# Optimization experiments

Hardware: AMD Instinct MI355X
Metric: run time of the kernel (lower is better)

The kernel has to match this reference:

```python
import jax, jax.numpy as jnp
import numpy as np

M_CHK, N_VAR, DV = 576, 1152, 3  # (3,x)-regular-column LDPC, rate 1/2
PI = 3.1415926


def _build_bp_matrices():
    """Vectorized replica of GetMatrixForBPNet (same math, no Python O(E^2) loops)."""
    rng = np.random.default_rng(0)
    H = np.zeros((M_CHK, N_VAR), np.float32)
    rows = np.argsort(rng.random((N_VAR, M_CHK)), axis=1)[:, :DV]  # DV distinct rows per column
    H[rows.ravel(), np.repeat(np.arange(N_VAR), DV)] = 1.0
    ii, jj = np.nonzero(H)                 # row-major edge list (sorted by row, then col)
    E = ii.size
    p_r2l = np.lexsort((ii, jj))           # Map_row_to_line: col-major position -> row-major index
    p_l2r = np.argsort(p_r2l)              # Map_line_to_row: inverse permutation
    cols_cm = jj[p_r2l]                    # column of each edge in col-major ("line") order
    # variable-node sum excluding self, in col-major order, then permute row-major input -> col-major
    S_V = (cols_cm[:, None] == cols_cm[None, :]).astype(np.float32)
    np.fill_diagonal(S_V, 0.0)
    H_sumV_to_C = np.zeros((E, E), np.float32)
    H_sumV_to_C[:, p_r2l] = S_V
    # check-node sum excluding self, in row-major order, then permute col-major input -> row-major
    S_C = (ii[:, None] == ii[None, :]).astype(np.float32)
    np.fill_diagonal(S_C, 0.0)
    H_sumC_to_V = np.zeros((E, E), np.float32)
    H_sumC_to_V[:, p_l2r] = S_C
    # llr -> per-edge init (col-major order)
    H_x_to_xe0 = np.zeros((E, N_VAR), np.float32)
    H_x_to_xe0[np.arange(E), cols_cm] = 1.0
    # per-variable sum of final edge messages (row-major input -> col-major sum)
    A = (np.arange(N_VAR)[:, None] == cols_cm[None, :]).astype(np.float32)
    H_xe_v_sumc_to_y = np.zeros((N_VAR, E), np.float32)
    H_xe_v_sumc_to_y[:, p_r2l] = A
    return H_x_to_xe0, H_sumC_to_V, H_sumV_to_C, H_xe_v_sumc_to_y


def setup_inputs() -> dict:
    key = jax.random.key(0)
    H_x_to_xe0, H_sumC_to_V, H_sumV_to_C, H_xe_v_sumc_to_y = _build_bp_matrices()
    llr_in = 2.0 * jax.random.normal(key, (16, N_VAR), dtype=jnp.float32)
    return {
        "llr_in": llr_in,
        "H_x_to_xe0": jnp.asarray(H_x_to_xe0),
        "H_sumC_to_V": jnp.asarray(H_sumC_to_V),
        "H_sumV_to_C": jnp.asarray(H_sumV_to_C),
        "H_xe_v_sumc_to_y": jnp.asarray(H_xe_v_sumc_to_y),
        "bp_iter_num": 8,
    }


def _one_bp_iteration(xe_v2c, xe_0, H_sumC_to_V, H_sumV_to_C):
    xe_tanh = jnp.tanh(xe_v2c / 2.0)
    sgn = jnp.sign(xe_tanh)
    # log-domain product over check-node neighbors (excluding self) via complex log trick
    sum_log_img = H_sumC_to_V @ ((1.0 - sgn) * (0.5 * PI))
    sum_log_real = H_sumC_to_V @ jnp.log(1e-8 + jnp.abs(xe_tanh))
    xe_product = jnp.exp(sum_log_real) * jnp.cos(sum_log_img)  # Re(exp(r + i*theta))
    xe_pd = xe_product + jnp.sign(xe_product) * (-2e-7)
    # 2 * atanh(x) with the module's custom atanh = 0.5*log((1+x)/(1-x+1e-10))
    xe_v_sumc = jnp.log((1.0 + xe_pd) / (1.0 - xe_pd + 1e-10))
    xe_c_sumv = xe_0 + H_sumV_to_C @ xe_v_sumc
    return xe_v_sumc, xe_c_sumv


def reference(llr_in, H_x_to_xe0, H_sumC_to_V, H_sumV_to_C, H_xe_v_sumc_to_y, bp_iter_num):
    llr_t = llr_in.T                      # [n, batch]
    xe_0 = H_x_to_xe0 @ llr_t             # [E, batch]
    xe_v2c = xe_0
    for _ in range(bp_iter_num - 1):
        _, xe_v2c = _one_bp_iteration(xe_v2c, xe_0, H_sumC_to_V, H_sumV_to_C)
    xe_v_sumc, _ = _one_bp_iteration(xe_v2c, xe_0, H_sumC_to_V, H_sumV_to_C)
    bp_out_llr = llr_t + H_xe_v_sumc_to_y @ xe_v_sumc
    dec_out = (1 - jnp.sign(bp_out_llr).astype(jnp.int32)) // 2
    return dec_out.T
```

## Files before the change

kernel.cpp:

```cpp
#include <hip/hip_runtime.h>

#define NV 1152
#define MC 576
#define NE 3456
#define RPG 36
#define GRP 16
#define EMAX 384

__global__ __launch_bounds__(256) void k_tri(const float* __restrict__ Hy,
                                             int* __restrict__ tri) {
    __shared__ int found[8];
    __shared__ int cnt;
    const int v = blockIdx.x, t = threadIdx.x;
    if (t == 0) cnt = 0;
    __syncthreads();
    const float4* row4 = (const float4*)(Hy + (size_t)v * NE);
    for (int c = t; c < 864; c += 256) {
        float4 q = row4[c];
        if (q.x != 0.0f) { int s = atomicAdd(&cnt, 1); if (s < 8) found[s] = 4 * c; }
        if (q.y != 0.0f) { int s = atomicAdd(&cnt, 1); if (s < 8) found[s] = 4 * c + 1; }
        if (q.z != 0.0f) { int s = atomicAdd(&cnt, 1); if (s < 8) found[s] = 4 * c + 2; }
        if (q.w != 0.0f) { int s = atomicAdd(&cnt, 1); if (s < 8) found[s] = 4 * c + 3; }
    }
    __syncthreads();
    if (t == 0) {
        int a = found[0], b = found[1], c = found[2];
        int lo = min(a, min(b, c));
        int hi = max(a, max(b, c));
        int mid = a + b + c - lo - hi;
        tri[3 * v] = lo; tri[3 * v + 1] = mid; tri[3 * v + 2] = hi;
    }
}

__global__ __launch_bounds__(1024) void k_build(const float* __restrict__ Hc,
                                                const int* __restrict__ tri,
                                                unsigned short* __restrict__ pl2r_g,
                                                int* __restrict__ rs_g) {
    __shared__ unsigned short pl2r[NE];
    __shared__ unsigned short flg[NE];
    __shared__ int wtot[16];
    const int t = threadIdx.x;
    const int lane = t & 63, wid = t >> 6;
    for (int r = t; r < MC + 1; r += 1024) rs_g[r] = NE;
    for (int e = t; e < NE; e += 1024) pl2r[tri[e]] = (unsigned short)e;
    __syncthreads();
    for (int a = t; a < NE; a += 1024) {
        int fl = 0;
        if (a > 0) fl = (Hc[(size_t)(a - 1) * NE + (int)pl2r[a]] == 0.0f) ? 1 : 0;
        flg[a] = (unsigned short)fl;
        pl2r_g[a] = pl2r[a];
    }
    __syncthreads();
    int inc[4];
    int run = 0;
    const int base4 = t * 4;
    #pragma unroll
    for (int k = 0; k < 4; k++) {
        int idx = base4 + k;
        run += (idx < NE) ? (int)flg[idx] : 0;
        inc[k] = run;
    }
    int x = run;
    #pragma unroll
    for (int d = 1; d < 64; d <<= 1) {
        int y = __shfl_up(x, d, 64);
        if (lane >= d) x += y;
    }
    if (lane == 63) wtot[wid] = x;
    __syncthreads();
    if (t < 16) {
        int v = wtot[t];
        #pragma unroll
        for (int d = 1; d < 16; d <<= 1) {
            int y = __shfl_up(v, d, 16);
            if (t >= d) v += y;
        }
        wtot[t] = v;
    }
    __syncthreads();
    const int prefix = ((wid > 0) ? wtot[wid - 1] : 0) + (x - run);
    #pragma unroll
    for (int k = 0; k < 4; k++) {
        int idx = base4 + k;
        if (idx < NE) {
            int rid = prefix + inc[k];
            if (idx == 0 || flg[idx]) rs_g[rid] = idx;
        }
    }
}

__global__ __launch_bounds__(256) void k_iter(const float* __restrict__ llr,
                                              const unsigned short* __restrict__ p_l2r,
                                              const int* __restrict__ rs,
                                              const float* __restrict__ msg_in,
                                              float* __restrict__ msg_out,
                                              int first) {
    __shared__ float2 lrli[EMAX];
    __shared__ unsigned short eloc[EMAX];
    __shared__ unsigned char rloc[EMAX];
    __shared__ int rsl[RPG + 1];
    const int g = blockIdx.x, b = blockIdx.y, t = threadIdx.x;
    if (t <= RPG) rsl[t] = rs[g * RPG + t];
    __syncthreads();
    const int s0 = rsl[0], s1 = rsl[RPG];
    for (int a = s0 + t; a < s1; a += 256) {
        int la = a - s0;
        int lo = 0, hi = RPG - 1;
        while (lo < hi) { int mid = (lo + hi + 1) >> 1; if (rsl[mid] <= a) lo = mid; else hi = mid - 1; }
        rloc[la] = (unsigned char)lo;
        int e = p_l2r[a];
        eloc[la] = (unsigned short)e;
        int v = e / 3;
        float xv = llr[b * NV + v];
        if (!first) {
            int v3 = 3 * v, r_ = e - v3;
            int o1 = v3 + ((r_ == 0) ? 1 : 0);
            int o2 = v3 + ((r_ == 2) ? 1 : 2);
            xv = xv + (msg_in[b * NE + o1] + msg_in[b * NE + o2]);
        }
        float tv = tanhf(0.5f * xv);
        float sgn = (tv > 0.0f) ? 1.0f : ((tv < 0.0f) ? -1.0f : 0.0f);
        lrli[la] = make_float2(logf(1e-8f + fabsf(tv)),
                               (1.0f - sgn) * 1.5707963f);
    }
    __syncthreads();
    for (int a = s0 + t; a < s1; a += 256) {
        int la = a - s0;
        int r = rloc[la];
        int js = rsl[r] - s0, je = rsl[r + 1] - s0;
        float slr = 0.0f, sli = 0.0f;
        for (int j = js; j < je; ++j) {
            if (j != la) { float2 q = lrli[j]; slr += q.x; sli += q.y; }
        }
        float p = expf(slr) * cosf(sli);
        float ps = (p > 0.0f) ? 1.0f : ((p < 0.0f) ? -1.0f : 0.0f);
        float pd = p - 2e-7f * ps;
        msg_out[b * NE + eloc[la]] = logf((1.0f + pd) / ((1.0f - pd) + 1e-10f));
    }
}

__global__ void k_out(const float* __restrict__ llr, const float* __restrict__ msg,
                      int* __restrict__ out, int n) {
    int i = blockIdx.x * 256 + threadIdx.x;
    if (i >= n) return;
    int b = i / NV, v = i - b * NV;
    const float* m = msg + (size_t)b * NE + 3 * v;
    float S = (m[0] + m[1]) + m[2];
    out[i] = ((llr[i] + S) < 0.0f) ? 1 : 0;
}

extern "C" void kernel_launch(void* const* d_in, const int* in_sizes, int n_in,
                              void* d_out, int out_size, void* d_ws, size_t ws_size,
                              hipStream_t stream) {
    const float* llr_in = (const float*)d_in[0];
    const float* Hc2v   = (const float*)d_in[2];
    const float* Hy     = (const float*)d_in[4];
    const int batch = in_sizes[0] / NV;
    int* tri = (int*)d_ws;
    int* rs  = tri + NE;
    float* msgA = (float*)(rs + 580);
    float* msgB = msgA + (size_t)batch * NE;
    unsigned short* pl2r = (unsigned short*)(msgB + (size_t)batch * NE);

    hipLaunchKernelGGL(k_tri, dim3(NV), dim3(256), 0, stream, Hy, tri);
    hipLaunchKernelGGL(k_build, dim3(1), dim3(1024), 0, stream, Hc2v, tri, pl2r, rs);
    hipLaunchKernelGGL(k_iter, dim3(GRP, batch), dim3(256), 0, stream,
                       llr_in, pl2r, rs, msgA, msgA, 1);
    float* bufs[2] = { msgA, msgB };
    for (int it = 1; it < 8; ++it) {
        float* in  = bufs[(it + 1) & 1];
        float* out = bufs[it & 1];
        hipLaunchKernelGGL(k_iter, dim3(GRP, batch), dim3(256), 0, stream,
                           llr_in, pl2r, rs, in, out, 0);
    }
    const int n = batch * NV;
    hipLaunchKernelGGL(k_out, dim3((n + 255) / 256), dim3(256), 0, stream,
                       llr_in, msgB, (int*)d_out, n);
}
```

Baseline: 180.3 us.

## Fuse all BP stages into one cooperative persistent kernel with grid barriers

Replaces the separate launches (edge-finding, structure build, eight iteration launches and output) with a single cooperative kernel of GRP*batch blocks. Grid-wide atomic barriers separate the setup phases, and per-batch counters synchronise the 16 blocks that share a codeword between iterations. The per-block edge metadata and llr values are loaded into shared memory once and reused across all iterations. This removes about ten kernel launch gaps but adds spin-barrier overhead, a memset, and serialised setup, since only 256 blocks now scan the large Hy matrix.

```diff
diff --git a/kernel.cpp b/kernel.cpp
--- a/kernel.cpp
+++ b/kernel.cpp
@@ -7,99 +7,111 @@
 #define GRP 16
 #define EMAX 384
 
-__global__ __launch_bounds__(256) void k_tri(const float* __restrict__ Hy,
-                                             int* __restrict__ tri) {
-    __shared__ int found[8];
-    __shared__ int cnt;
-    const int v = blockIdx.x, t = threadIdx.x;
-    if (t == 0) cnt = 0;
+__device__ __forceinline__ void wait_bar(int* c, int target) {
     __syncthreads();
-    const float4* row4 = (const float4*)(Hy + (size_t)v * NE);
-    for (int c = t; c < 864; c += 256) {
-        float4 q = row4[c];
-        if (q.x != 0.0f) { int s = atomicAdd(&cnt, 1); if (s < 8) found[s] = 4 * c; }
-        if (q.y != 0.0f) { int s = atomicAdd(&cnt, 1); if (s < 8) found[s] = 4 * c + 1; }
-        if (q.z != 0.0f) { int s = atomicAdd(&cnt, 1); if (s < 8) found[s] = 4 * c + 2; }
-        if (q.w != 0.0f) { int s = atomicAdd(&cnt, 1); if (s < 8) found[s] = 4 * c + 3; }
+    if (threadIdx.x == 0) {
+        __hip_atomic_fetch_add(c, 1, __ATOMIC_ACQ_REL, __HIP_MEMORY_SCOPE_AGENT);
+        while (__hip_atomic_load(c, __ATOMIC_ACQUIRE, __HIP_MEMORY_SCOPE_AGENT) < target)
+            __builtin_amdgcn_s_sleep(1);
     }
     __syncthreads();
-    if (t == 0) {
-        int a = found[0], b = found[1], c = found[2];
-        int lo = min(a, min(b, c));
-        int hi = max(a, max(b, c));
-        int mid = a + b + c - lo - hi;
-        tri[3 * v] = lo; tri[3 * v + 1] = mid; tri[3 * v + 2] = hi;
-    }
 }
 
-__global__ __launch_bounds__(1024) void k_build(const float* __restrict__ Hc,
-                                                const int* __restrict__ tri,
-                                                unsigned short* __restrict__ pl2r_g,
-                                                int* __restrict__ rs_g) {
-    __shared__ unsigned short pl2r[NE];
-    __shared__ unsigned short flg[NE];
-    __shared__ int wtot[16];
-    const int t = threadIdx.x;
-    const int lane = t & 63, wid = t >> 6;
-    for (int r = t; r < MC + 1; r += 1024) rs_g[r] = NE;
-    for (int e = t; e < NE; e += 1024) pl2r[tri[e]] = (unsigned short)e;
-    __syncthreads();
-    for (int a = t; a < NE; a += 1024) {
-        int fl = 0;
-        if (a > 0) fl = (Hc[(size_t)(a - 1) * NE + (int)pl2r[a]] == 0.0f) ? 1 : 0;
-        flg[a] = (unsigned short)fl;
-        pl2r_g[a] = pl2r[a];
-    }
-    __syncthreads();
-    int inc[4];
-    int run = 0;
-    const int base4 = t * 4;
-    #pragma unroll
-    for (int k = 0; k < 4; k++) {
-        int idx = base4 + k;
-        run += (idx < NE) ? (int)flg[idx] : 0;
-        inc[k] = run;
-    }
-    int x = run;
-    #pragma unroll
-    for (int d = 1; d < 64; d <<= 1) {
-        int y = __shfl_up(x, d, 64);
-        if (lane >= d) x += y;
-    }
-    if (lane == 63) wtot[wid] = x;
-    __syncthreads();
-    if (t < 16) {
-        int v = wtot[t];
-        #pragma unroll
-        for (int d = 1; d < 16; d <<= 1) {
-            int y = __shfl_up(v, d, 16);
-            if (t >= d) v += y;
-        }
-        wtot[t] = v;
-    }
-    __syncthreads();
-    const int prefix = ((wid > 0) ? wtot[wid - 1] : 0) + (x - run);
-    #pragma unroll
-    for (int k = 0; k < 4; k++) {
-        int idx = base4 + k;
-        if (idx < NE) {
-            int rid = prefix + inc[k];
-            if (idx == 0 || flg[idx]) rs_g[rid] = idx;
-        }
-    }
-}
+#define GCNT(i)     (cnt + (i) * 16)
+#define BCNT(b, it) (cnt + (3 + (b) * 8 + (it)) * 16)
 
-__global__ __launch_bounds__(256) void k_iter(const float* __restrict__ llr,
-                                              const unsigned short* __restrict__ p_l2r,
-                                              const int* __restrict__ rs,
-                                              const float* __restrict__ msg_in,
-                                              float* __restrict__ msg_out,
-                                              int first) {
+__global__ __launch_bounds__(256) void k_bp(const float* __restrict__ llr,
+                                            const float* __restrict__ Hc,
+                                            const float* __restrict__ Hy,
+                                            unsigned short* __restrict__ pl2r,
+                                            int* __restrict__ rs,
+                                            unsigned char* __restrict__ flg,
+                                            float* __restrict__ msgA,
+                                            float* __restrict__ msgB,
+                                            int* __restrict__ cnt,
+                                            int* __restrict__ out) {
+    const int bid = blockIdx.x, t = threadIdx.x;
+    const int nblk = gridDim.x;
+    __shared__ int found[8];
+    __shared__ int fcnt;
+    __shared__ int wtot[4];
+    __shared__ int rsl[RPG + 1];
     __shared__ float2 lrli[EMAX];
     __shared__ unsigned short eloc[EMAX];
     __shared__ unsigned char rloc[EMAX];
-    __shared__ int rsl[RPG + 1];
-    const int g = blockIdx.x, b = blockIdx.y, t = threadIdx.x;
+    __shared__ float xb[EMAX];
+
+    for (int v = bid; v < NV; v += nblk) {
+        if (t == 0) fcnt = 0;
+        __syncthreads();
+        const float4* row4 = (const float4*)(Hy + (size_t)v * NE);
+        for (int c4 = t; c4 < 864; c4 += 256) {
+            float4 q = row4[c4];
+            if (q.x != 0.0f) { int s = atomicAdd(&fcnt, 1); if (s < 8) found[s] = 4 * c4; }
+            if (q.y != 0.0f) { int s = atomicAdd(&fcnt, 1); if (s < 8) found[s] = 4 * c4 + 1; }
+            if (q.z != 0.0f) { int s = atomicAdd(&fcnt, 1); if (s < 8) found[s] = 4 * c4 + 2; }
+            if (q.w != 0.0f) { int s = atomicAdd(&fcnt, 1); if (s < 8) found[s] = 4 * c4 + 3; }
+        }
+        __syncthreads();
+        if (t == 0) {
+            int a = found[0], b2 = found[1], c2 = found[2];
+            int lo = min(a, min(b2, c2));
+            int hi = max(a, max(b2, c2));
+            int mid = a + b2 + c2 - lo - hi;
+            pl2r[lo]  = (unsigned short)(3 * v);
+            pl2r[mid] = (unsigned short)(3 * v + 1);
+            pl2r[hi]  = (unsigned short)(3 * v + 2);
+        }
+        __syncthreads();
+    }
+    wait_bar(GCNT(0), nblk);
+
+    {
+        int gt = bid * 256 + t;
+        if (gt <= MC) rs[gt] = NE;
+        if (gt < NE) {
+            int fl = 0;
+            if (gt > 0) fl = (Hc[(size_t)(gt - 1) * NE + (int)pl2r[gt]] == 0.0f) ? 1 : 0;
+            flg[gt] = (unsigned char)fl;
+        }
+    }
+    wait_bar(GCNT(1), nblk);
+
+    if (bid == 0) {
+        const int lane = t & 63, wid = t >> 6;
+        int inc[14];
+        int run = 0;
+        const int base = t * 14;
+        #pragma unroll
+        for (int k = 0; k < 14; k++) {
+            int idx = base + k;
+            run += (idx < NE) ? (int)flg[idx] : 0;
+            inc[k] = run;
+        }
+        int x = run;
+        #pragma unroll
+        for (int d = 1; d < 64; d <<= 1) {
+            int y = __shfl_up(x, d, 64);
+            if (lane >= d) x += y;
+        }
+        if (lane == 63) wtot[wid] = x;
+        __syncthreads();
+        if (t == 0) {
+            int s = 0;
+            #pragma unroll
+            for (int w = 0; w < 4; w++) { int v = wtot[w]; wtot[w] = s; s += v; }
+        }
+        __syncthreads();
+        const int prefix = wtot[wid] + (x - run);
+        #pragma unroll
+        for (int k = 0; k < 14; k++) {
+            int idx = base + k;
+            if (idx < NE && (idx == 0 || flg[idx])) rs[prefix + inc[k]] = idx;
+        }
+    }
+    wait_bar(GCNT(2), nblk);
+
+    const int g = bid & 15, b = bid >> 4;
     if (t <= RPG) rsl[t] = rs[g * RPG + t];
     __syncthreads();
     const int s0 = rsl[0], s1 = rsl[RPG];
@@ -108,45 +120,54 @@
         int lo = 0, hi = RPG - 1;
         while (lo < hi) { int mid = (lo + hi + 1) >> 1; if (rsl[mid] <= a) lo = mid; else hi = mid - 1; }
         rloc[la] = (unsigned char)lo;
-        int e = p_l2r[a];
+        int e = pl2r[a];
         eloc[la] = (unsigned short)e;
-        int v = e / 3;
-        float xv = llr[b * NV + v];
-        if (!first) {
-            int v3 = 3 * v, r_ = e - v3;
-            int o1 = v3 + ((r_ == 0) ? 1 : 0);
-            int o2 = v3 + ((r_ == 2) ? 1 : 2);
-            xv = xv + (msg_in[b * NE + o1] + msg_in[b * NE + o2]);
-        }
-        float tv = tanhf(0.5f * xv);
-        float sgn = (tv > 0.0f) ? 1.0f : ((tv < 0.0f) ? -1.0f : 0.0f);
-        lrli[la] = make_float2(logf(1e-8f + fabsf(tv)),
-                               (1.0f - sgn) * 1.5707963f);
+        xb[la] = llr[b * NV + e / 3];
     }
     __syncthreads();
-    for (int a = s0 + t; a < s1; a += 256) {
-        int la = a - s0;
-        int r = rloc[la];
-        int js = rsl[r] - s0, je = rsl[r + 1] - s0;
-        float slr = 0.0f, sli = 0.0f;
-        for (int j = js; j < je; ++j) {
-            if (j != la) { float2 q = lrli[j]; slr += q.x; sli += q.y; }
+
+    for (int it = 0; it < 8; ++it) {
+        const float* mi = (it & 1) ? msgA : msgB;
+        float* mo       = (it & 1) ? msgB : msgA;
+        for (int a = s0 + t; a < s1; a += 256) {
+            int la = a - s0;
+            int e = eloc[la];
+            float xv = xb[la];
+            if (it > 0) {
+                int v3 = 3 * (e / 3), r_ = e - v3;
+                int o1 = v3 + ((r_ == 0) ? 1 : 0);
+                int o2 = v3 + ((r_ == 2) ? 1 : 2);
+                xv = xv + (mi[b * NE + o1] + mi[b * NE + o2]);
+            }
+            float tv = tanhf(0.5f * xv);
+            float sgn = (tv > 0.0f) ? 1.0f : ((tv < 0.0f) ? -1.0f : 0.0f);
+            lrli[la] = make_float2(logf(1e-8f + fabsf(tv)),
+                                   (1.0f - sgn) * 1.5707963f);
         }
-        float p = expf(slr) * cosf(sli);
-        float ps = (p > 0.0f) ? 1.0f : ((p < 0.0f) ? -1.0f : 0.0f);
-        float pd = p - 2e-7f * ps;
-        msg_out[b * NE + eloc[la]] = logf((1.0f + pd) / ((1.0f - pd) + 1e-10f));
+        __syncthreads();
+        for (int a = s0 + t; a < s1; a += 256) {
+            int la = a - s0;
+            int r = rloc[la];
+            int js = rsl[r] - s0, je = rsl[r + 1] - s0;
+            float slr = 0.0f, sli = 0.0f;
+            for (int j = js; j < je; ++j) {
+                if (j != la) { float2 q = lrli[j]; slr += q.x; sli += q.y; }
+            }
+            float p = expf(slr) * cosf(sli);
+            float ps = (p > 0.0f) ? 1.0f : ((p < 0.0f) ? -1.0f : 0.0f);
+            float pd = p - 2e-7f * ps;
+            mo[b * NE + eloc[la]] = logf((1.0f + pd) / ((1.0f - pd) + 1e-10f));
+        }
+        wait_bar(BCNT(b, it), GRP);
     }
-}
 
-__global__ void k_out(const float* __restrict__ llr, const float* __restrict__ msg,
-                      int* __restrict__ out, int n) {
-    int i = blockIdx.x * 256 + threadIdx.x;
-    if (i >= n) return;
-    int b = i / NV, v = i - b * NV;
-    const float* m = msg + (size_t)b * NE + 3 * v;
-    float S = (m[0] + m[1]) + m[2];
-    out[i] = ((llr[i] + S) < 0.0f) ? 1 : 0;
+    if (t < 72) {
+        int v = g * 72 + t;
+        int i = b * NV + v;
+        const float* m = msgB + (size_t)b * NE + 3 * v;
+        float S = (m[0] + m[1]) + m[2];
+        out[i] = ((llr[i] + S) < 0.0f) ? 1 : 0;
+    }
 }
 
 extern "C" void kernel_launch(void* const* d_in, const int* in_sizes, int n_in,
@@ -156,24 +177,21 @@
     const float* Hc2v   = (const float*)d_in[2];
     const float* Hy     = (const float*)d_in[4];
     const int batch = in_sizes[0] / NV;
-    int* tri = (int*)d_ws;
-    int* rs  = tri + NE;
-    float* msgA = (float*)(rs + 580);
+
+    float* msgA = (float*)d_ws;
     float* msgB = msgA + (size_t)batch * NE;
-    unsigned short* pl2r = (unsigned short*)(msgB + (size_t)batch * NE);
+    int* rs = (int*)(msgB + (size_t)batch * NE);
+    unsigned short* pl2r = (unsigned short*)(rs + 580);
+    unsigned char* flg = (unsigned char*)(pl2r + NE);
+    int* cnt = (int*)(flg + NE);
+    int* outp = (int*)d_out;
 
-    hipLaunchKernelGGL(k_tri, dim3(NV), dim3(256), 0, stream, Hy, tri);
-    hipLaunchKernelGGL(k_build, dim3(1), dim3(1024), 0, stream, Hc2v, tri, pl2r, rs);
-    hipLaunchKernelGGL(k_iter, dim3(GRP, batch), dim3(256), 0, stream,
-                       llr_in, pl2r, rs, msgA, msgA, 1);
-    float* bufs[2] = { msgA, msgB };
-    for (int it = 1; it < 8; ++it) {
-        float* in  = bufs[(it + 1) & 1];
-        float* out = bufs[it & 1];
-        hipLaunchKernelGGL(k_iter, dim3(GRP, batch), dim3(256), 0, stream,
-                           llr_in, pl2r, rs, in, out, 0);
-    }
-    const int n = batch * NV;
-    hipLaunchKernelGGL(k_out, dim3((n + 255) / 256), dim3(256), 0, stream,
-                       llr_in, msgB, (int*)d_out, n);
+    const int n_cnt = (3 + 8 * batch) * 16;
+    hipMemsetAsync(cnt, 0, n_cnt * sizeof(int), stream);
+
+    void* args[] = { (void*)&llr_in, (void*)&Hc2v, (void*)&Hy, (void*)&pl2r,
+                     (void*)&rs, (void*)&flg, (void*)&msgA, (void*)&msgB,
+                     (void*)&cnt, (void*)&outp };
+    hipLaunchCooperativeKernel((const void*)k_bp, dim3(GRP * batch), dim3(256),
+                               args, 0, stream);
 }
```

Result: slower. 338.3 us (+87.6%).

## Fuse all BP iterations and output into one per-batch persistent block

Applied to the files above, without the earlier changes.

Replaces the eight per-iteration k_iter launches plus k_out with a single k_main kernel where each block handles one batch row. All edge messages stay in shared memory across iterations, with block-wide barriers between the variable-node and check-node phases. k_tri now writes the inverse permutation directly, so k_build no longer scatters it. This removes launch overhead and global message round-trips, but only 16 blocks run (one per batch row), leaving most compute units idle.

```diff
diff --git a/kernel.cpp b/kernel.cpp
--- a/kernel.cpp
+++ b/kernel.cpp
@@ -3,52 +3,46 @@
 #define NV 1152
 #define MC 576
 #define NE 3456
-#define RPG 36
-#define GRP 16
-#define EMAX 384
 
 __global__ __launch_bounds__(256) void k_tri(const float* __restrict__ Hy,
-                                             int* __restrict__ tri) {
+                                             unsigned short* __restrict__ pl2r) {
     __shared__ int found[8];
-    __shared__ int cnt;
+    __shared__ int fcnt;
     const int v = blockIdx.x, t = threadIdx.x;
-    if (t == 0) cnt = 0;
+    if (t == 0) fcnt = 0;
     __syncthreads();
     const float4* row4 = (const float4*)(Hy + (size_t)v * NE);
-    for (int c = t; c < 864; c += 256) {
-        float4 q = row4[c];
-        if (q.x != 0.0f) { int s = atomicAdd(&cnt, 1); if (s < 8) found[s] = 4 * c; }
-        if (q.y != 0.0f) { int s = atomicAdd(&cnt, 1); if (s < 8) found[s] = 4 * c + 1; }
-        if (q.z != 0.0f) { int s = atomicAdd(&cnt, 1); if (s < 8) found[s] = 4 * c + 2; }
-        if (q.w != 0.0f) { int s = atomicAdd(&cnt, 1); if (s < 8) found[s] = 4 * c + 3; }
+    for (int c4 = t; c4 < 864; c4 += 256) {
+        float4 q = row4[c4];
+        if (q.x != 0.0f) { int s = atomicAdd(&fcnt, 1); if (s < 8) found[s] = 4 * c4; }
+        if (q.y != 0.0f) { int s = atomicAdd(&fcnt, 1); if (s < 8) found[s] = 4 * c4 + 1; }
+        if (q.z != 0.0f) { int s = atomicAdd(&fcnt, 1); if (s < 8) found[s] = 4 * c4 + 2; }
+        if (q.w != 0.0f) { int s = atomicAdd(&fcnt, 1); if (s < 8) found[s] = 4 * c4 + 3; }
     }
     __syncthreads();
     if (t == 0) {
-        int a = found[0], b = found[1], c = found[2];
-        int lo = min(a, min(b, c));
-        int hi = max(a, max(b, c));
-        int mid = a + b + c - lo - hi;
-        tri[3 * v] = lo; tri[3 * v + 1] = mid; tri[3 * v + 2] = hi;
+        int a = found[0], b2 = found[1], c2 = found[2];
+        int lo = min(a, min(b2, c2));
+        int hi = max(a, max(b2, c2));
+        int mid = a + b2 + c2 - lo - hi;
+        pl2r[lo]  = (unsigned short)(3 * v);
+        pl2r[mid] = (unsigned short)(3 * v + 1);
+        pl2r[hi]  = (unsigned short)(3 * v + 2);
     }
 }
 
 __global__ __launch_bounds__(1024) void k_build(const float* __restrict__ Hc,
-                                                const int* __restrict__ tri,
-                                                unsigned short* __restrict__ pl2r_g,
-                                                int* __restrict__ rs_g) {
-    __shared__ unsigned short pl2r[NE];
+                                                const unsigned short* __restrict__ pl2r,
+                                                int* __restrict__ rs) {
     __shared__ unsigned short flg[NE];
     __shared__ int wtot[16];
     const int t = threadIdx.x;
     const int lane = t & 63, wid = t >> 6;
-    for (int r = t; r < MC + 1; r += 1024) rs_g[r] = NE;
-    for (int e = t; e < NE; e += 1024) pl2r[tri[e]] = (unsigned short)e;
-    __syncthreads();
+    for (int r = t; r < MC + 1; r += 1024) rs[r] = NE;
     for (int a = t; a < NE; a += 1024) {
         int fl = 0;
         if (a > 0) fl = (Hc[(size_t)(a - 1) * NE + (int)pl2r[a]] == 0.0f) ? 1 : 0;
         flg[a] = (unsigned short)fl;
-        pl2r_g[a] = pl2r[a];
     }
     __syncthreads();
     int inc[4];
@@ -84,69 +78,70 @@
         int idx = base4 + k;
         if (idx < NE) {
             int rid = prefix + inc[k];
-            if (idx == 0 || flg[idx]) rs_g[rid] = idx;
+            if (idx == 0 || flg[idx]) rs[rid] = idx;
         }
     }
 }
 
-__global__ __launch_bounds__(256) void k_iter(const float* __restrict__ llr,
-                                              const unsigned short* __restrict__ p_l2r,
-                                              const int* __restrict__ rs,
-                                              const float* __restrict__ msg_in,
-                                              float* __restrict__ msg_out,
-                                              int first) {
-    __shared__ float2 lrli[EMAX];
-    __shared__ unsigned short eloc[EMAX];
-    __shared__ unsigned char rloc[EMAX];
-    __shared__ int rsl[RPG + 1];
-    const int g = blockIdx.x, b = blockIdx.y, t = threadIdx.x;
-    if (t <= RPG) rsl[t] = rs[g * RPG + t];
+__global__ __launch_bounds__(1024) void k_main(const float* __restrict__ llr,
+                                               const unsigned short* __restrict__ pl2r,
+                                               const int* __restrict__ rs,
+                                               int* __restrict__ out) {
+    __shared__ int rsl[MC + 1];
+    __shared__ unsigned short ecm[NE];
+    __shared__ unsigned short rloc[NE];
+    __shared__ float llr_s[NV];
+    __shared__ float msg[NE];
+    __shared__ float2 lrli[NE];
+    const int b = blockIdx.x, t = threadIdx.x;
+
+    for (int r = t; r < MC + 1; r += 1024) rsl[r] = rs[r];
+    for (int v = t; v < NV; v += 1024) llr_s[v] = llr[b * NV + v];
+    for (int a = t; a < NE; a += 1024) ecm[a] = pl2r[a];
     __syncthreads();
-    const int s0 = rsl[0], s1 = rsl[RPG];
-    for (int a = s0 + t; a < s1; a += 256) {
-        int la = a - s0;
-        int lo = 0, hi = RPG - 1;
+    for (int a = t; a < NE; a += 1024) {
+        int lo = 0, hi = MC - 1;
         while (lo < hi) { int mid = (lo + hi + 1) >> 1; if (rsl[mid] <= a) lo = mid; else hi = mid - 1; }
-        rloc[la] = (unsigned char)lo;
-        int e = p_l2r[a];
-        eloc[la] = (unsigned short)e;
-        int v = e / 3;
-        float xv = llr[b * NV + v];
-        if (!first) {
-            int v3 = 3 * v, r_ = e - v3;
-            int o1 = v3 + ((r_ == 0) ? 1 : 0);
-            int o2 = v3 + ((r_ == 2) ? 1 : 2);
-            xv = xv + (msg_in[b * NE + o1] + msg_in[b * NE + o2]);
-        }
-        float tv = tanhf(0.5f * xv);
-        float sgn = (tv > 0.0f) ? 1.0f : ((tv < 0.0f) ? -1.0f : 0.0f);
-        lrli[la] = make_float2(logf(1e-8f + fabsf(tv)),
-                               (1.0f - sgn) * 1.5707963f);
+        rloc[a] = (unsigned short)lo;
     }
     __syncthreads();
-    for (int a = s0 + t; a < s1; a += 256) {
-        int la = a - s0;
-        int r = rloc[la];
-        int js = rsl[r] - s0, je = rsl[r + 1] - s0;
-        float slr = 0.0f, sli = 0.0f;
-        for (int j = js; j < je; ++j) {
-            if (j != la) { float2 q = lrli[j]; slr += q.x; sli += q.y; }
+
+    for (int it = 0; it < 8; ++it) {
+        for (int a = t; a < NE; a += 1024) {
+            int e = ecm[a];
+            int v = e / 3;
+            float xv = llr_s[v];
+            if (it > 0) {
+                int v3 = 3 * v, r_ = e - v3;
+                int o1 = v3 + ((r_ == 0) ? 1 : 0);
+                int o2 = v3 + ((r_ == 2) ? 1 : 2);
+                xv = xv + (msg[o1] + msg[o2]);
+            }
+            float tv = tanhf(0.5f * xv);
+            float sgn = (tv > 0.0f) ? 1.0f : ((tv < 0.0f) ? -1.0f : 0.0f);
+            lrli[a] = make_float2(logf(1e-8f + fabsf(tv)),
+                                  (1.0f - sgn) * 1.5707963f);
         }
-        float p = expf(slr) * cosf(sli);
-        float ps = (p > 0.0f) ? 1.0f : ((p < 0.0f) ? -1.0f : 0.0f);
-        float pd = p - 2e-7f * ps;
-        msg_out[b * NE + eloc[la]] = logf((1.0f + pd) / ((1.0f - pd) + 1e-10f));
+        __syncthreads();
+        for (int a = t; a < NE; a += 1024) {
+            int r = rloc[a];
+            int js = rsl[r], je = rsl[r + 1];
+            float slr = 0.0f, sli = 0.0f;
+            for (int j = js; j < je; ++j) {
+                if (j != a) { float2 q = lrli[j]; slr += q.x; sli += q.y; }
+            }
+            float p = expf(slr) * cosf(sli);
+            float ps = (p > 0.0f) ? 1.0f : ((p < 0.0f) ? -1.0f : 0.0f);
+            float pd = p - 2e-7f * ps;
+            msg[ecm[a]] = logf((1.0f + pd) / ((1.0f - pd) + 1e-10f));
+        }
+        __syncthreads();
     }
-}
 
-__global__ void k_out(const float* __restrict__ llr, const float* __restrict__ msg,
-                      int* __restrict__ out, int n) {
-    int i = blockIdx.x * 256 + threadIdx.x;
-    if (i >= n) return;
-    int b = i / NV, v = i - b * NV;
-    const float* m = msg + (size_t)b * NE + 3 * v;
-    float S = (m[0] + m[1]) + m[2];
-    out[i] = ((llr[i] + S) < 0.0f) ? 1 : 0;
+    for (int v = t; v < NV; v += 1024) {
+        float S = (msg[3 * v] + msg[3 * v + 1]) + msg[3 * v + 2];
+        out[b * NV + v] = ((llr_s[v] + S) < 0.0f) ? 1 : 0;
+    }
 }
 
 extern "C" void kernel_launch(void* const* d_in, const int* in_sizes, int n_in,
@@ -156,24 +151,12 @@
     const float* Hc2v   = (const float*)d_in[2];
     const float* Hy     = (const float*)d_in[4];
     const int batch = in_sizes[0] / NV;
-    int* tri = (int*)d_ws;
-    int* rs  = tri + NE;
-    float* msgA = (float*)(rs + 580);
-    float* msgB = msgA + (size_t)batch * NE;
-    unsigned short* pl2r = (unsigned short*)(msgB + (size_t)batch * NE);
 
-    hipLaunchKernelGGL(k_tri, dim3(NV), dim3(256), 0, stream, Hy, tri);
-    hipLaunchKernelGGL(k_build, dim3(1), dim3(1024), 0, stream, Hc2v, tri, pl2r, rs);
-    hipLaunchKernelGGL(k_iter, dim3(GRP, batch), dim3(256), 0, stream,
-                       llr_in, pl2r, rs, msgA, msgA, 1);
-    float* bufs[2] = { msgA, msgB };
-    for (int it = 1; it < 8; ++it) {
-        float* in  = bufs[(it + 1) & 1];
-        float* out = bufs[it & 1];
-        hipLaunchKernelGGL(k_iter, dim3(GRP, batch), dim3(256), 0, stream,
-                           llr_in, pl2r, rs, in, out, 0);
-    }
-    const int n = batch * NV;
-    hipLaunchKernelGGL(k_out, dim3((n + 255) / 256), dim3(256), 0, stream,
-                       llr_in, msgB, (int*)d_out, n);
+    int* rs = (int*)d_ws;
+    unsigned short* pl2r = (unsigned short*)(rs + 580);
+
+    hipLaunchKernelGGL(k_tri, dim3(NV), dim3(256), 0, stream, Hy, pl2r);
+    hipLaunchKernelGGL(k_build, dim3(1), dim3(1024), 0, stream, Hc2v, pl2r, rs);
+    hipLaunchKernelGGL(k_main, dim3(batch), dim3(1024), 0, stream,
+                       llr_in, pl2r, rs, llr_in ? (int*)d_out : (int*)d_out);
 }
```

After: 195.3 us. 8.3% more time.
